# Kernel optimization log

Measured on AMD Instinct MI355X. Metric: run time of the kernel, lower is better.

Reference implementation:

```python
import jax, jax.numpy as jnp
from jax import lax
import numpy as np

N, C, T, V, P, O = 32, 64, 300, 25, 3, 128
STRIDE = 2
EPS = 1e-5


def setup_inputs() -> dict:
    key = jax.random.key(0)
    ks = jax.random.split(key, 8)
    x = jax.random.normal(ks[0], (N, C, T, V), jnp.float32)
    A_parts = jax.random.uniform(ks[1], (P, V, V), jnp.float32)
    edge_importance = jnp.ones((P,), jnp.float32)
    gcn_w = jax.random.normal(ks[2], (O, C), jnp.float32) * 0.05
    gcn_b = jax.random.normal(ks[3], (O,), jnp.float32) * 0.05
    tcn_w = jax.random.normal(ks[4], (O, O, 9, 1), jnp.float32) * 0.02
    tcn_b = jax.random.normal(ks[5], (O,), jnp.float32) * 0.05
    bn_gamma = jnp.ones((O,), jnp.float32)
    bn_beta = jnp.zeros((O,), jnp.float32)
    res_w = jax.random.normal(ks[6], (O, C), jnp.float32) * 0.05
    res_b = jax.random.normal(ks[7], (O,), jnp.float32) * 0.05
    return {"x": x, "A_parts": A_parts, "edge_importance": edge_importance,
            "gcn_w": gcn_w, "gcn_b": gcn_b, "tcn_w": tcn_w, "tcn_b": tcn_b,
            "bn_gamma": bn_gamma, "bn_beta": bn_beta, "res_w": res_w, "res_b": res_b}


def reference(x, A_parts, edge_importance, gcn_w, gcn_b, tcn_w, tcn_b,
              bn_gamma, bn_beta, res_w, res_b):
    # Fused P-partition aggregation: sum_p (ei_p * A_p) applied once.
    A_sum = jnp.einsum('pvw,p->vw', A_parts, edge_importance)  # [V, V]
    agg = jnp.einsum('nctv,vw->nctw', x, A_sum)                # [N, C, T, V]
    # 1x1 gcn conv == channel matmul
    x_gcn = jnp.einsum('nctv,oc->notv', agg, gcn_w) + gcn_b[None, :, None, None]
    # temporal conv: kernel (9,1), stride (2,1), pad (4,0)
    x_tcn = lax.conv_general_dilated(
        x_gcn, tcn_w, window_strides=(STRIDE, 1), padding=((4, 4), (0, 0)),
        dimension_numbers=('NCHW', 'OIHW', 'NCHW'))
    x_tcn = x_tcn + tcn_b[None, :, None, None]
    # BatchNorm (training mode: batch statistics, biased variance)
    mean = jnp.mean(x_tcn, axis=(0, 2, 3), keepdims=True)
    var = jnp.var(x_tcn, axis=(0, 2, 3), keepdims=True)
    x_bn = (x_tcn - mean) * lax.rsqrt(var + EPS)
    x_bn = x_bn * bn_gamma[None, :, None, None] + bn_beta[None, :, None, None]
    # residual: 1x1 conv, stride (2,1) == temporal subsample + channel matmul
    x_sub = x[:, :, ::STRIDE, :]
    res = jnp.einsum('nctv,oc->notv', x_sub, res_w) + res_b[None, :, None, None]
    return jax.nn.relu(x_bn + res)
```

## Files before the change

kernel.cpp:

```cpp
#include <hip/hip_runtime.h>
#include <hip/hip_bf16.h>

typedef unsigned short u16;
typedef unsigned int   u32;

#define NB 32
#define CC 64
#define TT 300
#define VV 25
#define OO 128
#define TO 150
#define KT 9
#define MM 7500
#define MT 59
#define M2 3750

typedef short s8v  __attribute__((ext_vector_type(8)));
typedef float f4v  __attribute__((ext_vector_type(4)));
typedef u16  h4v  __attribute__((ext_vector_type(4)));
typedef u16  h8v  __attribute__((ext_vector_type(8)));

__device__ __forceinline__ float b2f(u16 u){
  union { u32 i; float f; } c; c.i = ((u32)u) << 16; return c.f;
}
__device__ __forceinline__ u16 f2b(float f){
  __hip_bfloat16 h = __float2bfloat16(f);
  return *reinterpret_cast<u16*>(&h);
}
__device__ __forceinline__ void async16(const void* g, void* l){
  __builtin_amdgcn_global_load_lds((const __attribute__((address_space(1))) u32*)g,
                                   (__attribute__((address_space(3))) u32*)l, 16, 0, 0);
}

__global__ __launch_bounds__(256) void k_prep(const float* __restrict__ Ap, const float* __restrict__ ei,
                                              const float* __restrict__ tw, const float* __restrict__ gw,
                                              const float* __restrict__ rw,
                                              float* __restrict__ Asum, float* __restrict__ zbuf,
                                              u16* __restrict__ Wq2, u16* __restrict__ gwb,
                                              u16* __restrict__ rwb){
  int idx = blockIdx.x * 256 + threadIdx.x;
  if (idx < VV*VV){
    float s = 0.f;
    for (int p = 0; p < 3; ++p) s += ei[p] * Ap[p*VV*VV + idx];
    Asum[idx] = s;
  }
  if (idx >= 640 && idx < 768) zbuf[idx - 640] = 0.f;
  int w = idx - 1024;
  if (w >= 0 && w < 18*OO*64){
    int kc = w >> 13;
    int r  = w & 8191;
    int o  = r >> 6;
    int j  = r & 63;
    int k  = kc >> 1;
    int i  = (kc & 1)*64 + j;
    Wq2[w] = f2b(tw[o*(OO*KT) + i*KT + k]);
  }
  int w2 = idx - 148480;
  if (w2 >= 0 && w2 < OO*CC) gwb[w2] = f2b(gw[w2]);
  int w3 = idx - 156672;
  if (w3 >= 0 && w3 < OO*CC) rwb[w3] = f2b(rw[w3]);
}

__global__ __launch_bounds__(256, 4) void k_gcnm(const float* __restrict__ x, const float* __restrict__ Asum,
                                                 const u16* __restrict__ gwb, const float* __restrict__ gb,
                                                 u16* __restrict__ xg){
  __shared__ __align__(16) u16 A_lds[128*64];
  __shared__ __align__(16) u16 B_lds[128*64];
  int bx = blockIdx.x;
  int n  = bx / MT;
  int m0 = (bx % MT) * 128;
  int t0 = m0 / VV, r0 = m0 % VV;
  int tid = threadIdx.x;
  int lane = tid & 63, wv = tid >> 6;
  int wm = (wv & 1) * 64, wo = (wv >> 1) * 64;
  int lr = lane & 15, lq = lane >> 4;

  {
    const u32* g32 = (const u32*)gwb;
    u32* b32 = (u32*)B_lds;
    for (int s = tid; s < 4096; s += 256){
      int row = s >> 5, col = s & 31;
      int g = col >> 2, c2 = col & 3;
      b32[row*32 + ((g ^ (row & 7))*4 + c2)] = g32[s];
    }
  }

  s8v bfw[2];
  #pragma unroll
  for (int wt = 0; wt < 2; ++wt){
    u16 tmp[8];
    int w = lr + 16*wt;
    #pragma unroll
    for (int j = 0; j < 8; ++j){
      int v = lq*8 + j;
      tmp[j] = (w < VV && v < VV) ? f2b(Asum[v*VV + w]) : (u16)0;
    }
    bfw[wt] = *(s8v*)tmp;
  }

  #pragma unroll
  for (int tt = 0; tt < 7; ++tt){
    int tau = tt*4 + wv;
    int it = tau >> 2, ct = tau & 3;
    int t  = t0 + it;
    int c  = ct*16 + lr;
    const float* xp = x + ((size_t)(n*CC + c)*TT + t)*VV + lq*8;
    float4 xa = make_float4(0.f,0.f,0.f,0.f), xb = xa;
    float x24 = 0.f;
    if (t < TT){
      if (lq < 3){
        xa = *(const float4*)xp;
        xb = *(const float4*)(xp + 4);
      } else {
        x24 = xp[0];
      }
    }
    u16 pk[8];
    if (lq < 3){
      pk[0]=f2b(xa.x); pk[1]=f2b(xa.y); pk[2]=f2b(xa.z); pk[3]=f2b(xa.w);
      pk[4]=f2b(xb.x); pk[5]=f2b(xb.y); pk[6]=f2b(xb.z); pk[7]=f2b(xb.w);
    } else {
      pk[0]=f2b(x24); pk[1]=0; pk[2]=0; pk[3]=0; pk[4]=0; pk[5]=0; pk[6]=0; pk[7]=0;
    }
    s8v af = *(s8v*)pk;
    f4v d0 = (f4v)(0.f), d1 = (f4v)(0.f);
    d0 = __builtin_amdgcn_mfma_f32_16x16x32_bf16(af, bfw[0], d0, 0, 0, 0);
    d1 = __builtin_amdgcn_mfma_f32_16x16x32_bf16(af, bfw[1], d1, 0, 0, 0);
    int cb = ct*16 + lq*4;
    int g  = cb >> 3, co = cb & 7;
    int ml0 = it*VV + lr - r0;
    if (ml0 >= 0 && ml0 < 128){
      u16 q[4];
      #pragma unroll
      for (int rg = 0; rg < 4; ++rg) q[rg] = f2b(d0[rg]);
      *(h4v*)&A_lds[ml0*64 + ((g ^ (ml0 & 7))*8) + co] = *(h4v*)q;
    }
    int w1 = lr + 16;
    int ml1 = it*VV + w1 - r0;
    if (w1 < VV && ml1 >= 0 && ml1 < 128){
      u16 q[4];
      #pragma unroll
      for (int rg = 0; rg < 4; ++rg) q[rg] = f2b(d1[rg]);
      *(h4v*)&A_lds[ml1*64 + ((g ^ (ml1 & 7))*8) + co] = *(h4v*)q;
    }
  }
  __syncthreads();

  f4v acc[4][4];
  #pragma unroll
  for (int mi = 0; mi < 4; ++mi)
    #pragma unroll
    for (int ni = 0; ni < 4; ++ni) acc[mi][ni] = (f4v)(0.f);
  #pragma unroll
  for (int ks = 0; ks < 2; ++ks){
    int p = ((ks*4 + lq) ^ (lane & 7)) * 8;
    s8v af[4], bf[4];
    #pragma unroll
    for (int mi = 0; mi < 4; ++mi)
      af[mi] = *(const s8v*)&A_lds[(wm + mi*16 + lr)*64 + p];
    #pragma unroll
    for (int ni = 0; ni < 4; ++ni)
      bf[ni] = *(const s8v*)&B_lds[(wo + ni*16 + lr)*64 + p];
    #pragma unroll
    for (int mi = 0; mi < 4; ++mi)
      #pragma unroll
      for (int ni = 0; ni < 4; ++ni)
        acc[mi][ni] = __builtin_amdgcn_mfma_f32_16x16x32_bf16(af[mi], bf[ni], acc[mi][ni], 0, 0, 0);
  }

  float bias[4];
  #pragma unroll
  for (int ni = 0; ni < 4; ++ni) bias[ni] = gb[wo + ni*16 + lr];
  #pragma unroll
  for (int mi = 0; mi < 4; ++mi){
    int mr = m0 + wm + mi*16 + lq*4;
    #pragma unroll
    for (int ni = 0; ni < 4; ++ni){
      int o = wo + ni*16 + lr;
      #pragma unroll
      for (int rg = 0; rg < 4; ++rg){
        int m = mr + rg;
        if (m < MM)
          xg[((size_t)n*MM + m)*OO + o] = f2b(acc[mi][ni][rg] + bias[ni]);
      }
    }
  }
}

__global__ __launch_bounds__(512, 4) void k_tcnm(const u16* __restrict__ xg, const u16* __restrict__ Wq2,
                                                 const float* __restrict__ tb, const u16* __restrict__ zbuf,
                                                 u16* __restrict__ xt, float* __restrict__ psum,
                                                 float* __restrict__ psq){
  __shared__ __align__(16) u16 A_lds[2][128*64];
  __shared__ __align__(16) u16 B_lds[2][128*64];
  __shared__ float sredS[8][64];
  __shared__ float sredQ[8][64];
  int bx = blockIdx.x;
  int n  = bx / 30;
  int m0 = (bx % 30) * 128;
  int tid = threadIdx.x;
  int lane = tid & 63, wv = tid >> 6;
  int wm = (wv >> 1) * 32, wo = (wv & 1) * 64;
  int lr = lane & 15, lq = lane >> 4;

  int rlow = tid >> 3;
  int gsrc = (tid & 7) ^ (rlow & 7);
  int tid16 = tid * 16;
  int  tbse[2], vr[2]; bool vm[2];
  #pragma unroll
  for (int it = 0; it < 2; ++it){
    int m = m0 + it*64 + rlow;
    vm[it] = (m < M2);
    int t2 = m / VV, v = m - t2*VV;
    tbse[it] = 2*t2 - 4;
    vr[it] = v;
  }
  size_t basen = (size_t)n*MM*OO + (size_t)gsrc*8;

  f4v acc[2][4];
  #pragma unroll
  for (int mi = 0; mi < 2; ++mi)
    #pragma unroll
    for (int ni = 0; ni < 4; ++ni) acc[mi][ni] = (f4v)(0.f);

  auto stage = [&](int kc, int b){
    int k  = kc >> 1;
    int i0 = (kc & 1) * 64;
    const u16* wbase = Wq2 + kc*8192;
    char* Ab = (char*)(&A_lds[b][0]);
    char* Bb = (char*)(&B_lds[b][0]);
    #pragma unroll
    for (int it = 0; it < 2; ++it){
      int t = tbse[it] + k;
      const u16* ga = (vm[it] && t >= 0 && t < TT)
                      ? xg + basen + (size_t)(t*VV + vr[it])*OO + i0
                      : zbuf;
      async16(ga, Ab + it*8192 + tid16);
      async16(wbase + ((it*64 + rlow)*64 + gsrc*8), Bb + it*8192 + tid16);
    }
  };

  stage(0, 0);
  for (int kc = 0; kc < 18; ++kc){
    int cur = kc & 1;
    if (kc < 17){
      stage(kc + 1, cur ^ 1);
      asm volatile("s_waitcnt vmcnt(4)" ::: "memory");
    } else {
      asm volatile("s_waitcnt vmcnt(0)" ::: "memory");
    }
    __builtin_amdgcn_s_barrier();
    asm volatile("" ::: "memory");

    const u16* Ac = &A_lds[cur][0];
    const u16* Bc = &B_lds[cur][0];
    #pragma unroll
    for (int ks = 0; ks < 2; ++ks){
      int p = ((ks*4 + lq) ^ (lane & 7)) * 8;
      s8v af[2], bf[4];
      #pragma unroll
      for (int mi = 0; mi < 2; ++mi)
        af[mi] = *(const s8v*)&Ac[(wm + mi*16 + lr)*64 + p];
      #pragma unroll
      for (int ni = 0; ni < 4; ++ni)
        bf[ni] = *(const s8v*)&Bc[(wo + ni*16 + lr)*64 + p];
      #pragma unroll
      for (int mi = 0; mi < 2; ++mi)
        #pragma unroll
        for (int ni = 0; ni < 4; ++ni)
          acc[mi][ni] = __builtin_amdgcn_mfma_f32_16x16x32_bf16(af[mi], bf[ni], acc[mi][ni], 0, 0, 0);
    }
    asm volatile("s_waitcnt lgkmcnt(0)" ::: "memory");
    __builtin_amdgcn_s_barrier();
    asm volatile("" ::: "memory");
  }

  float bias[4];
  #pragma unroll
  for (int ni = 0; ni < 4; ++ni) bias[ni] = tb[wo + ni*16 + lr];
  float sni[4] = {0.f,0.f,0.f,0.f}, qni[4] = {0.f,0.f,0.f,0.f};
  #pragma unroll
  for (int mi = 0; mi < 2; ++mi){
    int mr = m0 + wm + mi*16 + lq*4;
    #pragma unroll
    for (int ni = 0; ni < 4; ++ni){
      int o = wo + ni*16 + lr;
      #pragma unroll
      for (int rg = 0; rg < 4; ++rg){
        int m = mr + rg;
        if (m < M2){
          float val = acc[mi][ni][rg] + bias[ni];
          xt[((size_t)n*M2 + m)*OO + o] = f2b(val);
          sni[ni] += val;
          qni[ni] += val*val;
        }
      }
    }
  }
  #pragma unroll
  for (int ni = 0; ni < 4; ++ni){
    float s = sni[ni], q = qni[ni];
    s += __shfl_xor(s, 16); s += __shfl_xor(s, 32);
    q += __shfl_xor(q, 16); q += __shfl_xor(q, 32);
    if (lane < 16){
      sredS[wv][ni*16 + lane] = s;
      sredQ[wv][ni*16 + lane] = q;
    }
  }
  __syncthreads();
  if (tid < 128){
    int o = tid, h = o >> 6, lo = o & 63;
    psum[(size_t)bx*128 + o] = (sredS[h][lo] + sredS[h+2][lo]) + (sredS[h+4][lo] + sredS[h+6][lo]);
  } else if (tid < 256){
    int o = tid - 128, h = o >> 6, lo = o & 63;
    psq [(size_t)bx*128 + o] = (sredQ[h][lo] + sredQ[h+2][lo]) + (sredQ[h+4][lo] + sredQ[h+6][lo]);
  }
}

__global__ __launch_bounds__(256) void k_stats2a(const float* __restrict__ psum, const float* __restrict__ psq,
                                                 float* __restrict__ ps2, float* __restrict__ pq2){
  __shared__ float bufS[256], bufQ[256];
  int tid = threadIdx.x, b = blockIdx.x;
  int o = tid & 127, h = tid >> 7;
  float s = 0.f, q = 0.f;
  for (int r = b*16 + h; r < b*16 + 16; r += 2){
    s += psum[(size_t)r*128 + o];
    q += psq [(size_t)r*128 + o];
  }
  bufS[tid] = s; bufQ[tid] = q;
  __syncthreads();
  if (tid < 128){
    ps2[(size_t)b*128 + o] = bufS[tid] + bufS[tid + 128];
    pq2[(size_t)b*128 + o] = bufQ[tid] + bufQ[tid + 128];
  }
}

__global__ __launch_bounds__(256) void k_stats2b(const float* __restrict__ ps2, const float* __restrict__ pq2,
                                                 const float* __restrict__ gamma, const float* __restrict__ beta,
                                                 float* __restrict__ stats){
  __shared__ float bufS[256], bufQ[256];
  int tid = threadIdx.x;
  int o = tid & 127, h = tid >> 7;
  float s = 0.f, q = 0.f;
  for (int b = h; b < 60; b += 2){
    s += ps2[(size_t)b*128 + o];
    q += pq2[(size_t)b*128 + o];
  }
  bufS[tid] = s; bufQ[tid] = q;
  __syncthreads();
  if (tid < 128){
    s = bufS[tid] + bufS[tid + 128];
    q = bufQ[tid] + bufQ[tid + 128];
    const float inv = 1.f / 120000.f;
    float mean = s * inv;
    float var  = q * inv - mean*mean;
    float sc = gamma[o] * rsqrtf(var + 1e-5f);
    stats[o]       = sc;
    stats[128 + o] = beta[o] - mean * sc;
  }
}

__global__ __launch_bounds__(256, 4) void k_resm(const float* __restrict__ x, const u16* __restrict__ rwb,
                                                 const float* __restrict__ rb, const u16* __restrict__ xt,
                                                 const float* __restrict__ stats, float* __restrict__ out){
  __shared__ __align__(16) u16 A_lds[128*64];
  __shared__ __align__(16) u16 B_lds[128*64];
  int bx = blockIdx.x;
  int n  = bx / 30;
  int m0 = (bx % 30) * 128;
  int t20 = m0 / VV, r0 = m0 % VV;
  int tid = threadIdx.x;
  int lane = tid & 63, wv = tid >> 6;
  int wm = (wv & 1) * 64, wo = (wv >> 1) * 64;
  int lr = lane & 15, lq = lane >> 4;

  {
    const u32* g32 = (const u32*)rwb;
    u32* b32 = (u32*)B_lds;
    for (int s = tid; s < 4096; s += 256){
      int row = s >> 5, col = s & 31;
      int g = col >> 2, c2 = col & 3;
      b32[row*32 + ((g ^ (row & 7))*4 + c2)] = g32[s];
    }
  }

  for (int task = tid; task < 8*7*VV; task += 256){
    int cg  = task / (7*VV);
    int rem = task - cg*(7*VV);
    int t2i = rem / VV, v = rem - t2i*VV;
    int t2 = t20 + t2i;
    int ml = t2i*VV + v - r0;
    if (ml >= 0 && ml < 128){
      u16 pk[8];
      if (t2 < TO){
        const float* xp = x + ((size_t)(n*CC + cg*8)*TT + 2*t2)*VV + v;
        #pragma unroll
        for (int cc = 0; cc < 8; ++cc) pk[cc] = f2b(xp[(size_t)cc*(TT*VV)]);
      } else {
        #pragma unroll
        for (int cc = 0; cc < 8; ++cc) pk[cc] = 0;
      }
      *(h8v*)&A_lds[ml*64 + ((cg ^ (ml & 7))*8)] = *(h8v*)pk;
    }
  }
  __syncthreads();

  f4v acc[4][4];
  #pragma unroll
  for (int mi = 0; mi < 4; ++mi)
    #pragma unroll
    for (int ni = 0; ni < 4; ++ni) acc[mi][ni] = (f4v)(0.f);
  #pragma unroll
  for (int ks = 0; ks < 2; ++ks){
    int p = ((ks*4 + lq) ^ (lane & 7)) * 8;
    s8v af[4], bf[4];
    #pragma unroll
    for (int mi = 0; mi < 4; ++mi)
      af[mi] = *(const s8v*)&A_lds[(wm + mi*16 + lr)*64 + p];
    #pragma unroll
    for (int ni = 0; ni < 4; ++ni)
      bf[ni] = *(const s8v*)&B_lds[(wo + ni*16 + lr)*64 + p];
    #pragma unroll
    for (int mi = 0; mi < 4; ++mi)
      #pragma unroll
      for (int ni = 0; ni < 4; ++ni)
        acc[mi][ni] = __builtin_amdgcn_mfma_f32_16x16x32_bf16(af[mi], bf[ni], acc[mi][ni], 0, 0, 0);
  }

  float sc[4], sb[4], rr[4];
  #pragma unroll
  for (int ni = 0; ni < 4; ++ni){
    int o = wo + ni*16 + lr;
    sc[ni] = stats[o]; sb[ni] = stats[128 + o]; rr[ni] = rb[o];
  }
  #pragma unroll
  for (int mi = 0; mi < 4; ++mi){
    int mb = m0 + wm + mi*16 + lq*4;
    #pragma unroll
    for (int ni = 0; ni < 4; ++ni){
      int o = wo + ni*16 + lr;
      size_t xb = ((size_t)n*M2 + mb)*OO + o;
      size_t ob = ((size_t)(n*OO + o))*M2 + mb;
      if (mb + 3 < M2){
        float r0_ = fmaxf(sc[ni]*b2f(xt[xb])        + sb[ni] + acc[mi][ni][0] + rr[ni], 0.f);
        float r1_ = fmaxf(sc[ni]*b2f(xt[xb + OO])   + sb[ni] + acc[mi][ni][1] + rr[ni], 0.f);
        float r2_ = fmaxf(sc[ni]*b2f(xt[xb + 2*OO]) + sb[ni] + acc[mi][ni][2] + rr[ni], 0.f);
        float r3_ = fmaxf(sc[ni]*b2f(xt[xb + 3*OO]) + sb[ni] + acc[mi][ni][3] + rr[ni], 0.f);
        *(float2*)&out[ob]     = make_float2(r0_, r1_);
        *(float2*)&out[ob + 2] = make_float2(r2_, r3_);
      } else {
        #pragma unroll
        for (int rg = 0; rg < 4; ++rg){
          int m = mb + rg;
          if (m < M2){
            float r = sc[ni]*b2f(xt[xb + (size_t)rg*OO]) + sb[ni] + acc[mi][ni][rg] + rr[ni];
            out[ob + rg] = fmaxf(r, 0.f);
          }
        }
      }
    }
  }
}

extern "C" void kernel_launch(void* const* d_in, const int* in_sizes, int n_in,
                              void* d_out, int out_size, void* d_ws, size_t ws_size,
                              hipStream_t stream) {
  const float* x     = (const float*)d_in[0];
  const float* Ap    = (const float*)d_in[1];
  const float* ei    = (const float*)d_in[2];
  const float* gw    = (const float*)d_in[3];
  const float* gb    = (const float*)d_in[4];
  const float* tw    = (const float*)d_in[5];
  const float* tb    = (const float*)d_in[6];
  const float* gamma = (const float*)d_in[7];
  const float* beta  = (const float*)d_in[8];
  const float* rw    = (const float*)d_in[9];
  const float* rb    = (const float*)d_in[10];
  float* out = (float*)d_out;

  char* ws = (char*)d_ws;
  float* Asum  = (float*)ws;
  float* zbuf  = (float*)(ws + 2560);
  u16*   Wq2   = (u16*)(ws + 4096);
  u16*   gwb   = (u16*)(ws + 299008);
  u16*   rwb   = (u16*)(ws + 315392);
  float* stats = (float*)(ws + 331776);
  float* psum  = (float*)(ws + 333824);
  float* psq   = (float*)(ws + 825344);
  float* ps2   = (float*)(ws + 1316864);
  float* pq2   = (float*)(ws + 1347584);
  u16*   xg    = (u16*)(ws + (2u<<20));
  u16*   xt    = (u16*)(ws + 63537152);

  k_prep   <<<dim3(644),    dim3(256), 0, stream>>>(Ap, ei, tw, gw, rw, Asum, zbuf, Wq2, gwb, rwb);
  k_gcnm   <<<dim3(NB*MT),  dim3(256), 0, stream>>>(x, Asum, gwb, gb, xg);
  k_tcnm   <<<dim3(NB*30),  dim3(512), 0, stream>>>(xg, Wq2, tb, (const u16*)zbuf, xt, psum, psq);
  k_stats2a<<<dim3(60),     dim3(256), 0, stream>>>(psum, psq, ps2, pq2);
  k_stats2b<<<dim3(1),      dim3(256), 0, stream>>>(ps2, pq2, gamma, beta, stats);
  k_resm   <<<dim3(NB*30),  dim3(256), 0, stream>>>(x, rwb, rb, xt, stats, out);
}
```

Baseline: 272.8 us.

## Halve tcn K-chunk to raise occupancy; stage residual output through LDS

The temporal conv GEMM now processes 36 K-steps of 32 channels instead of 18 steps of 64. The tcn weight layout and swizzle are reworked to match, and the LDS tile is halved so that 8 blocks per CU can be resident instead of 4. Separately, the residual/output kernel transposes results through an LDS buffer in two passes, so each row of the channel-major output is written with contiguous float2 stores instead of scattered ones. The trade-off is twice as many barriers per K loop in tcn and extra syncs and LDS traffic in the epilogue.

```diff
diff --git a/kernel.cpp b/kernel.cpp
--- a/kernel.cpp
+++ b/kernel.cpp
@@ -46,14 +46,14 @@
   }
   if (idx >= 640 && idx < 768) zbuf[idx - 640] = 0.f;
   int w = idx - 1024;
-  if (w >= 0 && w < 18*OO*64){
-    int kc = w >> 13;
-    int r  = w & 8191;
-    int o  = r >> 6;
-    int j  = r & 63;
-    int k  = kc >> 1;
-    int i  = (kc & 1)*64 + j;
-    Wq2[w] = f2b(tw[o*(OO*KT) + i*KT + k]);
+  if (w >= 0 && w < 36*OO*32){
+    int s  = w >> 12;
+    int r  = w & 4095;
+    int o  = r >> 5;
+    int j  = r & 31;
+    int k  = s >> 2;
+    int iq = s & 3;
+    Wq2[w] = f2b(tw[o*(OO*KT) + (iq*32 + j)*KT + k]);
   }
   int w2 = idx - 148480;
   if (w2 >= 0 && w2 < OO*CC) gwb[w2] = f2b(gw[w2]);
@@ -187,12 +187,12 @@
   }
 }
 
-__global__ __launch_bounds__(512, 4) void k_tcnm(const u16* __restrict__ xg, const u16* __restrict__ Wq2,
+__global__ __launch_bounds__(512, 8) void k_tcnm(const u16* __restrict__ xg, const u16* __restrict__ Wq2,
                                                  const float* __restrict__ tb, const u16* __restrict__ zbuf,
                                                  u16* __restrict__ xt, float* __restrict__ psum,
                                                  float* __restrict__ psq){
-  __shared__ __align__(16) u16 A_lds[2][128*64];
-  __shared__ __align__(16) u16 B_lds[2][128*64];
+  __shared__ __align__(16) u16 A_lds[2][128*32];
+  __shared__ __align__(16) u16 B_lds[2][128*32];
   __shared__ float sredS[8][64];
   __shared__ float sredQ[8][64];
   int bx = blockIdx.x;
@@ -203,19 +203,14 @@
   int wm = (wv >> 1) * 32, wo = (wv & 1) * 64;
   int lr = lane & 15, lq = lane >> 4;
 
-  int rlow = tid >> 3;
-  int gsrc = (tid & 7) ^ (rlow & 7);
+  int rlow = tid >> 2;
+  int gs   = ((tid & 3) ^ (rlow & 3)) * 8;
   int tid16 = tid * 16;
-  int  tbse[2], vr[2]; bool vm[2];
-  #pragma unroll
-  for (int it = 0; it < 2; ++it){
-    int m = m0 + it*64 + rlow;
-    vm[it] = (m < M2);
-    int t2 = m / VV, v = m - t2*VV;
-    tbse[it] = 2*t2 - 4;
-    vr[it] = v;
-  }
-  size_t basen = (size_t)n*MM*OO + (size_t)gsrc*8;
+  int m = m0 + rlow;
+  bool vmv = (m < M2);
+  int t2v = m / VV, vrv = m - t2v*VV;
+  int tb2 = 2*t2v - 4;
+  size_t basen = (size_t)n*MM*OO + gs;
 
   f4v acc[2][4];
   #pragma unroll
@@ -223,29 +218,25 @@
     #pragma unroll
     for (int ni = 0; ni < 4; ++ni) acc[mi][ni] = (f4v)(0.f);
 
-  auto stage = [&](int kc, int b){
-    int k  = kc >> 1;
-    int i0 = (kc & 1) * 64;
-    const u16* wbase = Wq2 + kc*8192;
-    char* Ab = (char*)(&A_lds[b][0]);
-    char* Bb = (char*)(&B_lds[b][0]);
-    #pragma unroll
-    for (int it = 0; it < 2; ++it){
-      int t = tbse[it] + k;
-      const u16* ga = (vm[it] && t >= 0 && t < TT)
-                      ? xg + basen + (size_t)(t*VV + vr[it])*OO + i0
-                      : zbuf;
-      async16(ga, Ab + it*8192 + tid16);
-      async16(wbase + ((it*64 + rlow)*64 + gsrc*8), Bb + it*8192 + tid16);
-    }
+  auto stage = [&](int s, int b){
+    int k  = s >> 2;
+    int iq = s & 3;
+    int t  = tb2 + k;
+    const u16* ga = (vmv && t >= 0 && t < TT)
+                    ? xg + basen + (size_t)(t*VV + vrv)*OO + iq*32
+                    : zbuf;
+    async16(ga, (char*)(&A_lds[b][0]) + tid16);
+    async16(Wq2 + (size_t)s*4096 + rlow*32 + gs, (char*)(&B_lds[b][0]) + tid16);
   };
 
+  int pA = (lq ^ (lr & 3)) * 8;
+
   stage(0, 0);
-  for (int kc = 0; kc < 18; ++kc){
-    int cur = kc & 1;
-    if (kc < 17){
-      stage(kc + 1, cur ^ 1);
-      asm volatile("s_waitcnt vmcnt(4)" ::: "memory");
+  for (int s = 0; s < 36; ++s){
+    int cur = s & 1;
+    if (s < 35){
+      stage(s + 1, cur ^ 1);
+      asm volatile("s_waitcnt vmcnt(2)" ::: "memory");
     } else {
       asm volatile("s_waitcnt vmcnt(0)" ::: "memory");
     }
@@ -254,22 +245,19 @@
 
     const u16* Ac = &A_lds[cur][0];
     const u16* Bc = &B_lds[cur][0];
-    #pragma unroll
-    for (int ks = 0; ks < 2; ++ks){
-      int p = ((ks*4 + lq) ^ (lane & 7)) * 8;
-      s8v af[2], bf[4];
-      #pragma unroll
-      for (int mi = 0; mi < 2; ++mi)
-        af[mi] = *(const s8v*)&Ac[(wm + mi*16 + lr)*64 + p];
+    s8v af[2], bf[4];
+    #pragma unroll
+    for (int mi = 0; mi < 2; ++mi)
+      af[mi] = *(const s8v*)&Ac[(wm + mi*16 + lr)*32 + pA];
+    #pragma unroll
+    for (int ni = 0; ni < 4; ++ni)
+      bf[ni] = *(const s8v*)&Bc[(wo + ni*16 + lr)*32 + pA];
+    #pragma unroll
+    for (int mi = 0; mi < 2; ++mi)
       #pragma unroll
       for (int ni = 0; ni < 4; ++ni)
-        bf[ni] = *(const s8v*)&Bc[(wo + ni*16 + lr)*64 + p];
-      #pragma unroll
-      for (int mi = 0; mi < 2; ++mi)
-        #pragma unroll
-        for (int ni = 0; ni < 4; ++ni)
-          acc[mi][ni] = __builtin_amdgcn_mfma_f32_16x16x32_bf16(af[mi], bf[ni], acc[mi][ni], 0, 0, 0);
-    }
+        acc[mi][ni] = __builtin_amdgcn_mfma_f32_16x16x32_bf16(af[mi], bf[ni], acc[mi][ni], 0, 0, 0);
+
     asm volatile("s_waitcnt lgkmcnt(0)" ::: "memory");
     __builtin_amdgcn_s_barrier();
     asm volatile("" ::: "memory");
@@ -287,10 +275,10 @@
       int o = wo + ni*16 + lr;
       #pragma unroll
       for (int rg = 0; rg < 4; ++rg){
-        int m = mr + rg;
-        if (m < M2){
+        int mm = mr + rg;
+        if (mm < M2){
           float val = acc[mi][ni][rg] + bias[ni];
-          xt[((size_t)n*M2 + m)*OO + o] = f2b(val);
+          xt[((size_t)n*M2 + mm)*OO + o] = f2b(val);
           sni[ni] += val;
           qni[ni] += val*val;
         }
@@ -363,8 +351,10 @@
 __global__ __launch_bounds__(256, 4) void k_resm(const float* __restrict__ x, const u16* __restrict__ rwb,
                                                  const float* __restrict__ rb, const u16* __restrict__ xt,
                                                  const float* __restrict__ stats, float* __restrict__ out){
-  __shared__ __align__(16) u16 A_lds[128*64];
-  __shared__ __align__(16) u16 B_lds[128*64];
+  __shared__ __align__(16) char smem[64*130*4];
+  u16* A_lds = (u16*)smem;
+  u16* B_lds = A_lds + 128*64;
+  float* tbuf = (float*)smem;
   int bx = blockIdx.x;
   int n  = bx / 30;
   int m0 = (bx % 30) * 128;
@@ -433,31 +423,44 @@
     int o = wo + ni*16 + lr;
     sc[ni] = stats[o]; sb[ni] = stats[128 + o]; rr[ni] = rb[o];
   }
-  #pragma unroll
-  for (int mi = 0; mi < 4; ++mi){
-    int mb = m0 + wm + mi*16 + lq*4;
-    #pragma unroll
-    for (int ni = 0; ni < 4; ++ni){
-      int o = wo + ni*16 + lr;
-      size_t xb = ((size_t)n*M2 + mb)*OO + o;
-      size_t ob = ((size_t)(n*OO + o))*M2 + mb;
-      if (mb + 3 < M2){
-        float r0_ = fmaxf(sc[ni]*b2f(xt[xb])        + sb[ni] + acc[mi][ni][0] + rr[ni], 0.f);
-        float r1_ = fmaxf(sc[ni]*b2f(xt[xb + OO])   + sb[ni] + acc[mi][ni][1] + rr[ni], 0.f);
-        float r2_ = fmaxf(sc[ni]*b2f(xt[xb + 2*OO]) + sb[ni] + acc[mi][ni][2] + rr[ni], 0.f);
-        float r3_ = fmaxf(sc[ni]*b2f(xt[xb + 3*OO]) + sb[ni] + acc[mi][ni][3] + rr[ni], 0.f);
-        *(float2*)&out[ob]     = make_float2(r0_, r1_);
-        *(float2*)&out[ob + 2] = make_float2(r2_, r3_);
-      } else {
+
+  #pragma unroll
+  for (int pass = 0; pass < 2; ++pass){
+    __syncthreads();
+    if ((wv >> 1) == pass){
+      #pragma unroll
+      for (int mi = 0; mi < 4; ++mi){
+        int mb   = m0 + wm + mi*16 + lq*4;
+        int mloc = wm + mi*16 + lq*4;
         #pragma unroll
-        for (int rg = 0; rg < 4; ++rg){
-          int m = mb + rg;
-          if (m < M2){
-            float r = sc[ni]*b2f(xt[xb + (size_t)rg*OO]) + sb[ni] + acc[mi][ni][rg] + rr[ni];
-            out[ob + rg] = fmaxf(r, 0.f);
+        for (int ni = 0; ni < 4; ++ni){
+          int o    = wo + ni*16 + lr;
+          int oloc = ni*16 + lr;
+          size_t xb = ((size_t)n*M2 + mb)*OO + o;
+          float v2[4];
+          #pragma unroll
+          for (int rg = 0; rg < 4; ++rg){
+            float val = 0.f;
+            if (mb + rg < M2)
+              val = fmaxf(sc[ni]*b2f(xt[xb + (size_t)rg*OO]) + sb[ni] + acc[mi][ni][rg] + rr[ni], 0.f);
+            v2[rg] = val;
           }
+          *(float2*)&tbuf[oloc*130 + mloc]     = make_float2(v2[0], v2[1]);
+          *(float2*)&tbuf[oloc*130 + mloc + 2] = make_float2(v2[2], v2[3]);
         }
       }
+    }
+    __syncthreads();
+    #pragma unroll
+    for (int it = 0; it < 16; ++it){
+      int row = it*4 + (tid >> 6);
+      int c2  = (tid & 63) * 2;
+      int o   = pass*64 + row;
+      int mg  = m0 + c2;
+      size_t ob = ((size_t)(n*OO + o))*M2 + mg;
+      float2 vv = *(float2*)&tbuf[row*130 + c2];
+      if (mg + 1 < M2)      *(float2*)&out[ob] = vv;
+      else if (mg < M2)     out[ob] = vv.x;
     }
   }
 }
```

Measured after the change: 283.7 us. 4.0% more time.

## Stage residual epilogue through LDS for coalesced stores; swizzle tcn block order

Applied to the files above, without the earlier changes.

The residual/output kernel now writes its fused BN+residual+ReLU results into a padded LDS tile, one half of the output channels per pass. All threads then write contiguous float2 runs along the time-vertex axis, replacing the strided per-lane float2 stores to the NCHW output. Separately, the temporal-conv kernel remaps block indices with an interleave so that neighbouring hardware blocks cover different batches and tiles, and it indexes the partial-statistics buffers by that logical block. The store path gains two extra barriers, and LDS is reused after the MFMA loop.

```diff
diff --git a/kernel.cpp b/kernel.cpp
--- a/kernel.cpp
+++ b/kernel.cpp
@@ -196,8 +196,9 @@
   __shared__ float sredS[8][64];
   __shared__ float sredQ[8][64];
   int bx = blockIdx.x;
-  int n  = bx / 30;
-  int m0 = (bx % 30) * 128;
+  int lg = ((bx & 7) * 120) + (bx >> 3);
+  int n  = lg / 30;
+  int m0 = (lg % 30) * 128;
   int tid = threadIdx.x;
   int lane = tid & 63, wv = tid >> 6;
   int wm = (wv >> 1) * 32, wo = (wv & 1) * 64;
@@ -287,10 +288,10 @@
       int o = wo + ni*16 + lr;
       #pragma unroll
       for (int rg = 0; rg < 4; ++rg){
-        int m = mr + rg;
-        if (m < M2){
+        int mm = mr + rg;
+        if (mm < M2){
           float val = acc[mi][ni][rg] + bias[ni];
-          xt[((size_t)n*M2 + m)*OO + o] = f2b(val);
+          xt[((size_t)n*M2 + mm)*OO + o] = f2b(val);
           sni[ni] += val;
           qni[ni] += val*val;
         }
@@ -310,10 +311,10 @@
   __syncthreads();
   if (tid < 128){
     int o = tid, h = o >> 6, lo = o & 63;
-    psum[(size_t)bx*128 + o] = (sredS[h][lo] + sredS[h+2][lo]) + (sredS[h+4][lo] + sredS[h+6][lo]);
+    psum[(size_t)lg*128 + o] = (sredS[h][lo] + sredS[h+2][lo]) + (sredS[h+4][lo] + sredS[h+6][lo]);
   } else if (tid < 256){
     int o = tid - 128, h = o >> 6, lo = o & 63;
-    psq [(size_t)bx*128 + o] = (sredQ[h][lo] + sredQ[h+2][lo]) + (sredQ[h+4][lo] + sredQ[h+6][lo]);
+    psq [(size_t)lg*128 + o] = (sredQ[h][lo] + sredQ[h+2][lo]) + (sredQ[h+4][lo] + sredQ[h+6][lo]);
   }
 }
 
@@ -363,8 +364,10 @@
 __global__ __launch_bounds__(256, 4) void k_resm(const float* __restrict__ x, const u16* __restrict__ rwb,
                                                  const float* __restrict__ rb, const u16* __restrict__ xt,
                                                  const float* __restrict__ stats, float* __restrict__ out){
-  __shared__ __align__(16) u16 A_lds[128*64];
-  __shared__ __align__(16) u16 B_lds[128*64];
+  __shared__ __align__(16) char smem[64*130*4];
+  u16* A_lds = (u16*)smem;
+  u16* B_lds = A_lds + 128*64;
+  float* tbuf = (float*)smem;
   int bx = blockIdx.x;
   int n  = bx / 30;
   int m0 = (bx % 30) * 128;
@@ -433,31 +436,44 @@
     int o = wo + ni*16 + lr;
     sc[ni] = stats[o]; sb[ni] = stats[128 + o]; rr[ni] = rb[o];
   }
-  #pragma unroll
-  for (int mi = 0; mi < 4; ++mi){
-    int mb = m0 + wm + mi*16 + lq*4;
-    #pragma unroll
-    for (int ni = 0; ni < 4; ++ni){
-      int o = wo + ni*16 + lr;
-      size_t xb = ((size_t)n*M2 + mb)*OO + o;
-      size_t ob = ((size_t)(n*OO + o))*M2 + mb;
-      if (mb + 3 < M2){
-        float r0_ = fmaxf(sc[ni]*b2f(xt[xb])        + sb[ni] + acc[mi][ni][0] + rr[ni], 0.f);
-        float r1_ = fmaxf(sc[ni]*b2f(xt[xb + OO])   + sb[ni] + acc[mi][ni][1] + rr[ni], 0.f);
-        float r2_ = fmaxf(sc[ni]*b2f(xt[xb + 2*OO]) + sb[ni] + acc[mi][ni][2] + rr[ni], 0.f);
-        float r3_ = fmaxf(sc[ni]*b2f(xt[xb + 3*OO]) + sb[ni] + acc[mi][ni][3] + rr[ni], 0.f);
-        *(float2*)&out[ob]     = make_float2(r0_, r1_);
-        *(float2*)&out[ob + 2] = make_float2(r2_, r3_);
-      } else {
+
+  #pragma unroll
+  for (int pass = 0; pass < 2; ++pass){
+    __syncthreads();
+    if ((wv >> 1) == pass){
+      #pragma unroll
+      for (int mi = 0; mi < 4; ++mi){
+        int mb   = m0 + wm + mi*16 + lq*4;
+        int mloc = wm + mi*16 + lq*4;
         #pragma unroll
-        for (int rg = 0; rg < 4; ++rg){
-          int m = mb + rg;
-          if (m < M2){
-            float r = sc[ni]*b2f(xt[xb + (size_t)rg*OO]) + sb[ni] + acc[mi][ni][rg] + rr[ni];
-            out[ob + rg] = fmaxf(r, 0.f);
+        for (int ni = 0; ni < 4; ++ni){
+          int o    = wo + ni*16 + lr;
+          int oloc = ni*16 + lr;
+          size_t xb = ((size_t)n*M2 + mb)*OO + o;
+          float v2[4];
+          #pragma unroll
+          for (int rg = 0; rg < 4; ++rg){
+            float val = 0.f;
+            if (mb + rg < M2)
+              val = fmaxf(sc[ni]*b2f(xt[xb + (size_t)rg*OO]) + sb[ni] + acc[mi][ni][rg] + rr[ni], 0.f);
+            v2[rg] = val;
           }
+          *(float2*)&tbuf[oloc*130 + mloc]     = make_float2(v2[0], v2[1]);
+          *(float2*)&tbuf[oloc*130 + mloc + 2] = make_float2(v2[2], v2[3]);
         }
       }
+    }
+    __syncthreads();
+    #pragma unroll
+    for (int it = 0; it < 16; ++it){
+      int row = it*4 + (tid >> 6);
+      int c2  = (tid & 63) * 2;
+      int o   = pass*64 + row;
+      int mg  = m0 + c2;
+      size_t ob = ((size_t)(n*OO + o))*M2 + mg;
+      float2 vv = *(float2*)&tbuf[row*130 + c2];
+      if (mg + 1 < M2)      *(float2*)&out[ob] = vv;
+      else if (mg < M2)     out[ob] = vv.x;
     }
   }
 }
```

Measured after the change: 269.7 us. Within noise of the previous version (-1.2%).
